# Optimization experiments

Measured on AMD Instinct MI355X. Metric: run time of the kernel, lower is better.

Reference implementation:

```python
import jax, jax.numpy as jnp
import numpy as np

NH, HD = 12, 64          # heads, head dim (d_model=768)
SC = HD ** -0.5          # both Attention and CA_Attention use head_dim**-0.5


def patchify(x, p1, p2):
    # 'b c (h p1) (w p2) -> b (h w) (p1 p2 c)'
    B, C, H, W = x.shape
    h, w = H // p1, W // p2
    x = x.reshape(B, C, h, p1, w, p2).transpose(0, 2, 4, 3, 5, 1)  # b h w p1 p2 c
    return x.reshape(B, h * w, p1 * p2 * C)


def unpatchify(x, h, w, p1, p2, c):
    # 'b (h w) (p1 p2 c) -> b c (h p1) (w p2)'
    B = x.shape[0]
    x = x.reshape(B, h, w, p1, p2, c).transpose(0, 5, 1, 3, 2, 4)
    return x.reshape(B, c, h * p1, w * p2)


def ln(x, g, b):
    m = x.mean(-1, keepdims=True)
    v = ((x - m) ** 2).mean(-1, keepdims=True)
    return (x - m) / jnp.sqrt(v + 1e-5) * g + b


def setup_inputs() -> dict:
    key = jax.random.key(0)
    specs = [
        ('img_feats', (2, 32, 112, 112, 80)), ('txt', (2, 77, 768)),
        ('pe_w_ax', (1120, 768)), ('pe_b_ax', (768,)),
        ('pe_w_sag', (1120, 768)), ('pe_b_sag', (768,)),
        ('pe_w_cor', (1568, 768)), ('pe_b_cor', (768,)),
        ('pos_ax', (1, 256, 768)), ('pos_sag', (1, 256, 768)), ('pos_cor', (1, 256, 768)),
        ('qw', (768, 768)), ('kw', (768, 768)), ('vw', (768, 768)),
        ('pw', (768, 768)), ('pb', (768,)),
        ('caq_w', (768, 768)), ('caq_b', (768,)), ('cak_w', (768, 768)), ('cak_b', (768,)),
        ('cav_w', (768, 768)), ('cav_b', (768,)), ('cao_w', (768, 768)), ('cao_b', (768,)),
        ('mlp_w1', (768, 3072)), ('mlp_b1', (3072,)), ('mlp_w2', (3072, 768)), ('mlp_b2', (768,)),
        ('ow_ax', (768, 1120)), ('ob_ax', (1120,)),
        ('ow_sag', (768, 1120)), ('ob_sag', (1120,)),
        ('ow_cor', (768, 1568)), ('ob_cor', (1568,)),
    ]
    big = {'img_feats', 'txt', 'pos_ax', 'pos_sag', 'pos_cor'}
    out = {}
    for k, (n, s) in zip(jax.random.split(key, len(specs)), specs):
        scale = 1.0 if n in big else 0.02
        out[n] = jax.random.normal(k, s, jnp.float32) * scale
    out['view_w'] = jnp.ones((3,), jnp.float32)
    for n in ('n1_g', 'n2_g', 'n3_g'):
        out[n] = jnp.ones((768,), jnp.float32)
    for n in ('n1_b', 'n2_b', 'n3_b'):
        out[n] = jnp.zeros((768,), jnp.float32)
    return out


def reference(img_feats, txt, pe_w_ax, pe_b_ax, pe_w_sag, pe_b_sag, pe_w_cor, pe_b_cor,
              pos_ax, pos_sag, pos_cor, view_w, qw, kw, vw, pw, pb,
              caq_w, caq_b, cak_w, cak_b, cav_w, cav_b, cao_w, cao_b,
              n1_g, n1_b, n2_g, n2_b, n3_g, n3_b,
              mlp_w1, mlp_b1, mlp_w2, mlp_b2,
              ow_ax, ob_ax, ow_sag, ob_sag, ow_cor, ob_cor):

    def img_attn(t):
        B, N, C = t.shape
        q = (t @ qw).reshape(B, N, NH, HD)
        k = (t @ kw).reshape(B, N, NH, HD)
        v = (t @ vw).reshape(B, N, NH, HD)
        a = jax.nn.softmax(jnp.einsum('bnkc,bmkc->bknm', q, k) * SC, axis=-1)
        x = jnp.einsum('bknm,bmkc->bnkc', a, v).reshape(B, N, C)
        return x @ pw + pb

    def ca_attn(t, im):
        B, T, _ = t.shape
        N = im.shape[1]
        qh = (t @ caq_w + caq_b).reshape(B, T, NH, HD).transpose(0, 2, 1, 3)
        kh = (im @ cak_w + cak_b).reshape(B, N, NH, HD).transpose(0, 2, 1, 3)
        vh = (im @ cav_w + cav_b).reshape(B, N, NH, HD).transpose(0, 2, 1, 3)
        a = jax.nn.softmax(jnp.einsum('bhid,bhjd->bhij', qh, kh) * SC, axis=-1)
        # faithful to original einsum 'b h i j, b h j d -> b h j d' (sums over i)
        o = jnp.einsum('bhij,bhjd->bhjd', a, vh)
        o = o.transpose(0, 2, 1, 3).reshape(B, N, NH * HD)
        return o @ cao_w + cao_b

    def branch(v2d, pe_w, pe_b, pos, ow, ob, p1, p2):
        B, C, H, W = v2d.shape
        h, w = H // p1, W // p2
        q = patchify(v2d, p1, p2) @ pe_w + pe_b + pos
        q = ln(q, n1_g, n1_b)
        q = q + img_attn(q)
        q = ln(q, n2_g, n2_b)
        x = q + ca_attn(txt, q)
        x = x + (jax.nn.gelu(ln(x, n3_g, n3_b) @ mlp_w1 + mlp_b1, approximate=False) @ mlp_w2 + mlp_b2)
        return unpatchify(x @ ow + ob, h, w, p1, p2, C)

    # adaptive_avg_pool3d to size-1 along one axis == mean over that axis
    ax = img_feats.mean(2)    # (B,C,H,W)
    sag = img_feats.mean(3)   # (B,C,D,W)
    cor = img_feats.mean(4)   # (B,C,D,H)
    oax = branch(ax, pe_w_ax, pe_b_ax, pos_ax, ow_ax, ob_ax, 7, 5)
    osag = branch(sag, pe_w_sag, pe_b_sag, pos_sag, ow_sag, ob_sag, 7, 5)
    ocor = branch(cor, pe_w_cor, pe_b_cor, pos_cor, ow_cor, ob_cor, 7, 7)
    v3 = (view_w[0] * oax[:, :, None] + view_w[1] * osag[:, :, :, None]
          + view_w[2] * ocor[:, :, :, :, None])
    return img_feats + v3
```

## Files before the change

### kernel.cpp

```cpp
#include <hip/hip_runtime.h>
#include <math.h>

typedef __attribute__((ext_vector_type(8))) short s8;
typedef __attribute__((ext_vector_type(4))) float f4;
typedef unsigned short u16;

__device__ inline u16 f2bf(float f) {
    unsigned u = __float_as_uint(f);
    u += 0x7fffu + ((u >> 16) & 1u);
    return (u16)(u >> 16);
}
__device__ inline float bf2f(u16 x) {
    return __uint_as_float(((unsigned)x) << 16);
}

__global__ __launch_bounds__(256) void mean3_k(const float* __restrict__ img,
                                               float* __restrict__ axp,
                                               float* __restrict__ sag,
                                               float* __restrict__ cor) {
    __shared__ float sl[112*81];
    int blk = blockIdx.x;
    int dc = blk & 15, bc = blk >> 4;
    int d0 = dc * 7;
    int t = threadIdx.x;
    f4 axr[9];
    #pragma unroll
    for (int k = 0; k < 9; ++k) axr[k] = (f4){0.f,0.f,0.f,0.f};
    const float* base = img + (size_t)bc * 1003520 + (size_t)d0 * 8960;
    for (int sidx = 0; sidx < 7; ++sidx) {
        const f4* sp = reinterpret_cast<const f4*>(base + (size_t)sidx * 8960);
        #pragma unroll
        for (int k = 0; k < 9; ++k) {
            int q = t + k * 256;
            if (q < 2240) {
                f4 v = sp[q];
                axr[k] += v;
                int h = q / 20, w4 = q % 20;
                float* row = &sl[h * 81 + w4 * 4];
                row[0] = v[0]; row[1] = v[1]; row[2] = v[2]; row[3] = v[3];
            }
        }
        __syncthreads();
        if (t < 112) {
            float acc = 0.f;
            #pragma unroll 8
            for (int w = 0; w < 80; ++w) acc += sl[t * 81 + w];
            cor[((size_t)bc * 112 + d0 + sidx) * 112 + t] = acc * (1.f / 80.f);
        } else if (t < 192) {
            int w = t - 112;
            float acc = 0.f;
            #pragma unroll 8
            for (int h = 0; h < 112; ++h) acc += sl[h * 81 + w];
            sag[((size_t)bc * 112 + d0 + sidx) * 80 + w] = acc * (1.f / 112.f);
        }
        __syncthreads();
    }
    float* axo = axp + ((size_t)dc * 64 + bc) * 8960;
    #pragma unroll
    for (int k = 0; k < 9; ++k) {
        int q = t + k * 256;
        if (q < 2240) *reinterpret_cast<f4*>(axo + q * 4) = axr[k];
    }
}

__global__ void axred_k(const float* __restrict__ axp, float* __restrict__ ax) {
    int idx = blockIdx.x * 256 + threadIdx.x;
    if (idx >= 143360) return;
    f4 s = (f4){0.f,0.f,0.f,0.f};
    #pragma unroll
    for (int i = 0; i < 16; ++i)
        s += *reinterpret_cast<const f4*>(axp + (size_t)i * 573440 + (size_t)idx * 4);
    s *= (1.f / 112.f);
    *reinterpret_cast<f4*>(ax + (size_t)idx * 4) = s;
}

struct TT {
    const float* in[16];
    u16* out[16];
    int K[16];
    int N[16];
    int start[16];
};

__global__ __launch_bounds__(256) void transp_all(TT tab) {
    __shared__ float tl[32][33];
    int bid = blockIdx.x;
    int e = 0;
    #pragma unroll
    for (int i = 1; i < 16; ++i) if (bid >= tab.start[i]) e = i;
    const float* in = tab.in[e];
    u16* out = tab.out[e];
    int K = tab.K[e], N = tab.N[e];
    int tid = bid - tab.start[e];
    int nt = N >> 5;
    int k0 = (tid / nt) * 32, n0 = (tid % nt) * 32;
    int t = threadIdx.x;
    int r = t >> 5, c = t & 31;
    #pragma unroll
    for (int i = 0; i < 4; ++i) tl[r + i*8][c] = in[(long)(k0 + r + i*8)*N + n0 + c];
    __syncthreads();
    #pragma unroll
    for (int i = 0; i < 4; ++i) out[(long)(n0 + r + i*8)*K + k0 + c] = f2bf(tl[c][r + i*8]);
}

__global__ void misc_k(const float* __restrict__ txt, u16* __restrict__ txtb,
                       const float* __restrict__ cak_b, const float* __restrict__ cav_b,
                       float* __restrict__ kvb) {
    int idx = blockIdx.x*256 + threadIdx.x;
    if (idx < 118272) { txtb[idx] = f2bf(txt[idx]); return; }
    int i2 = idx - 118272;
    if (i2 < 768) kvb[i2] = cak_b[i2];
    else if (i2 < 1536) kvb[i2] = cav_b[i2 - 768];
}

__global__ __launch_bounds__(256) void patchify3_k(const float* __restrict__ m_ax,
                                                   const float* __restrict__ m_sag,
                                                   const float* __restrict__ m_cor,
                                                   u16* __restrict__ P0, u16* __restrict__ P1,
                                                   u16* __restrict__ P2) {
    __shared__ float sl[32][113];
    int br = blockIdx.y;
    int X = blockIdx.x;
    int b = X / 112, rem = X % 112;
    int hh = rem / 7, pp1 = rem % 7;
    const float* src; u16* dst; int Wt, p2, PD;
    if (br == 0)      { src = m_ax;  dst = P0; Wt = 80;  p2 = 5; PD = 1120; }
    else if (br == 1) { src = m_sag; dst = P1; Wt = 80;  p2 = 5; PD = 1120; }
    else              { src = m_cor; dst = P2; Wt = 112; p2 = 7; PD = 1568; }
    int t = threadIdx.x;
    int row = hh*7 + pp1;
    int wq = Wt >> 2;
    for (int i = t; i < 32*wq; i += 256) {
        int c = i / wq, w4 = i % wq;
        float4 v = *reinterpret_cast<const float4*>(
            src + ((size_t)(b*32 + c)*112 + row)*Wt + w4*4);
        sl[c][w4*4+0] = v.x; sl[c][w4*4+1] = v.y; sl[c][w4*4+2] = v.z; sl[c][w4*4+3] = v.w;
    }
    __syncthreads();
    int tot = 16 * p2 * 32;
    for (int o = t; o < tot; o += 256) {
        int ww = o / (p2*32), rest = o % (p2*32);
        int pp2 = rest >> 5, c = rest & 31;
        dst[((size_t)(b*256 + hh*16 + ww))*PD + (pp1*p2 + pp2)*32 + c]
            = f2bf(sl[c][ww*p2 + pp2]);
    }
}

__device__ inline void load_tile(const u16* __restrict__ P, int ld, int nrows, int K,
                                 int r0, int k0, int t, s8 v[4]) {
    #pragma unroll
    for (int i = 0; i < 4; ++i) {
        int chunk = t + i*256;
        int row = chunk >> 4, c8 = (chunk & 15) * 8;
        s8 x;
        #pragma unroll
        for (int q = 0; q < 8; ++q) x[q] = 0;
        if (r0 + row < nrows && k0 + c8 < K)
            x = *reinterpret_cast<const s8*>(P + (long)(r0 + row)*ld + k0 + c8);
        v[i] = x;
    }
}
__device__ inline void write_tile(u16 (*S)[136], int t, const s8 v[4]) {
    #pragma unroll
    for (int i = 0; i < 4; ++i) {
        int chunk = t + i*256;
        *reinterpret_cast<s8*>(&S[chunk >> 4][(chunk & 15)*8]) = v[i];
    }
}
__device__ inline void mfma_tile(const u16 (*As)[136], const u16 (*Bs)[136],
                                 int wr, int wc, int lane, f4 acc[2][2]) {
    int lrow = lane & 15;
    #pragma unroll
    for (int kh = 0; kh < 4; ++kh) {
        int lk = kh*32 + (lane >> 4) * 8;
        s8 af0 = *reinterpret_cast<const s8*>(&As[wr*32 + lrow][lk]);
        s8 af1 = *reinterpret_cast<const s8*>(&As[wr*32 + 16 + lrow][lk]);
        s8 bg0 = *reinterpret_cast<const s8*>(&Bs[wc*32 + lrow][lk]);
        s8 bg1 = *reinterpret_cast<const s8*>(&Bs[wc*32 + 16 + lrow][lk]);
        acc[0][0] = __builtin_amdgcn_mfma_f32_16x16x32_bf16(af0, bg0, acc[0][0], 0, 0, 0);
        acc[0][1] = __builtin_amdgcn_mfma_f32_16x16x32_bf16(af0, bg1, acc[0][1], 0, 0, 0);
        acc[1][0] = __builtin_amdgcn_mfma_f32_16x16x32_bf16(af1, bg0, acc[1][0], 0, 0, 0);
        acc[1][1] = __builtin_amdgcn_mfma_f32_16x16x32_bf16(af1, bg1, acc[1][1], 0, 0, 0);
    }
}

__global__ __launch_bounds__(256) void gemm_bf(
    const u16* __restrict__ A, const u16* __restrict__ Bt,
    float* __restrict__ Cf, u16* __restrict__ Cb,
    int M, int N, int K, int lda, int ldb, int ldc,
    const float* __restrict__ bias, const float* __restrict__ resid,
    int act, float cscale, int mode)
{
    __shared__ u16 As[2][64][136];
    __shared__ u16 Bs[2][64][136];
    const u16* Ab = A;
    const u16* Bb = Bt;
    long coff = 0;
    int z = blockIdx.z;
    if (mode == 1) {
        long o = (long)(z / 12) * 256 * lda + (long)(z % 12) * 64;
        Ab += o; Bb += o; coff = (long)z * 256 * ldc;
    } else if (mode == 2) {
        Ab += (long)z * 65536; Bb += (long)z * 16384;
        coff = (long)(z / 12) * 256 * ldc + (long)(z % 12) * 64;
    } else if (mode == 3) {
        int rowblk = z / 12, h = z % 12;
        Ab += (long)(rowblk & 1) * 77 * lda + (long)h * 64;
        Bb += (long)rowblk * 256 * ldb + (long)h * 64;
        coff = (long)z * 77 * 256;
    }
    int t = threadIdx.x;
    int m0 = blockIdx.y * 64, n0 = blockIdx.x * 64;
    int wave = t >> 6, lane = t & 63;
    int wr = wave >> 1, wc = wave & 1;
    f4 acc[2][2];
    #pragma unroll
    for (int m = 0; m < 2; ++m)
        #pragma unroll
        for (int n = 0; n < 2; ++n)
            #pragma unroll
            for (int r = 0; r < 4; ++r) acc[m][n][r] = 0.f;
    int nk = (K + 127) >> 7;
    s8 pa[4], pbv[4];
    load_tile(Ab, lda, M, K, m0, 0, t, pa);
    load_tile(Bb, ldb, N, K, n0, 0, t, pbv);
    write_tile(As[0], t, pa);
    write_tile(Bs[0], t, pbv);
    __syncthreads();
    for (int kt = 0; kt < nk; ++kt) {
        int cur = kt & 1;
        if (kt + 1 < nk) {
            load_tile(Ab, lda, M, K, m0, (kt+1) << 7, t, pa);
            load_tile(Bb, ldb, N, K, n0, (kt+1) << 7, t, pbv);
        }
        mfma_tile(As[cur], Bs[cur], wr, wc, lane, acc);
        if (kt + 1 < nk) {
            write_tile(As[cur^1], t, pa);
            write_tile(Bs[cur^1], t, pbv);
        }
        __syncthreads();
    }
    #pragma unroll
    for (int m = 0; m < 2; ++m) {
        int rbase = m0 + wr*32 + m*16 + (lane >> 4) * 4;
        #pragma unroll
        for (int n = 0; n < 2; ++n) {
            int col = n0 + wc*32 + n*16 + (lane & 15);
            if (col >= N) continue;
            #pragma unroll
            for (int r = 0; r < 4; ++r) {
                int row = rbase + r;
                if (row >= M) continue;
                float v = acc[m][n][r];
                if (bias)  v += bias[col];
                if (resid) v += resid[(long)row * ldc + col];
                if (act == 1) v = 0.5f * v * (1.0f + erff(v * 0.70710678118654752f));
                v *= cscale;
                long ci = coff + (long)row * ldc + col;
                if (Cf) Cf[ci] = v;
                if (Cb) Cb[ci] = f2bf(v);
            }
        }
    }
}

struct PeDesc {
    const u16* A[3];
    const u16* Bt[3];
    const float* bias[3];
    const float* pos[3];
    int K[3];
};

__global__ __launch_bounds__(256) void gemm_pe(PeDesc d, float* __restrict__ C) {
    __shared__ u16 As[2][64][136];
    __shared__ u16 Bs[2][64][136];
    int z = blockIdx.z;
    const u16* Ab = d.A[z];
    const u16* Bb = d.Bt[z];
    const float* bias = d.bias[z];
    const float* pos = d.pos[z];
    int K = d.K[z];
    int t = threadIdx.x;
    int m0 = blockIdx.y * 64, n0 = blockIdx.x * 64;
    int wave = t >> 6, lane = t & 63;
    int wr = wave >> 1, wc = wave & 1;
    f4 acc[2][2];
    #pragma unroll
    for (int m = 0; m < 2; ++m)
        #pragma unroll
        for (int n = 0; n < 2; ++n)
            #pragma unroll
            for (int r = 0; r < 4; ++r) acc[m][n][r] = 0.f;
    int nk = (K + 127) >> 7;
    s8 pa[4], pbv[4];
    load_tile(Ab, K, 512, K, m0, 0, t, pa);
    load_tile(Bb, K, 768, K, n0, 0, t, pbv);
    write_tile(As[0], t, pa);
    write_tile(Bs[0], t, pbv);
    __syncthreads();
    for (int kt = 0; kt < nk; ++kt) {
        int cur = kt & 1;
        if (kt + 1 < nk) {
            load_tile(Ab, K, 512, K, m0, (kt+1) << 7, t, pa);
            load_tile(Bb, K, 768, K, n0, (kt+1) << 7, t, pbv);
        }
        mfma_tile(As[cur], Bs[cur], wr, wc, lane, acc);
        if (kt + 1 < nk) {
            write_tile(As[cur^1], t, pa);
            write_tile(Bs[cur^1], t, pbv);
        }
        __syncthreads();
    }
    float* Cz = C + (long)z * 512 * 768;
    #pragma unroll
    for (int m = 0; m < 2; ++m) {
        int rbase = m0 + wr*32 + m*16 + (lane >> 4) * 4;
        #pragma unroll
        for (int n = 0; n < 2; ++n) {
            int col = n0 + wc*32 + n*16 + (lane & 15);
            #pragma unroll
            for (int r = 0; r < 4; ++r) {
                int row = rbase + r;
                float v = acc[m][n][r] + bias[col] + pos[(long)(row & 255)*768 + col];
                Cz[(long)row * 768 + col] = v;
            }
        }
    }
}

struct OwDesc {
    const u16* Bt[3];
    float* C[3];
    const float* bias[3];
    int N[3];
};

__global__ __launch_bounds__(256) void gemm_ow(OwDesc d, const u16* __restrict__ A) {
    int z = blockIdx.z;
    int N = d.N[z];
    int n0 = blockIdx.x * 64;
    if (n0 >= N) return;
    __shared__ u16 As[2][64][136];
    __shared__ u16 Bs[2][64][136];
    const u16* Ab = A + (long)z * 512 * 768;
    const u16* Bb = d.Bt[z];
    int t = threadIdx.x;
    int m0 = blockIdx.y * 64;
    int wave = t >> 6, lane = t & 63;
    int wr = wave >> 1, wc = wave & 1;
    f4 acc[2][2];
    #pragma unroll
    for (int m = 0; m < 2; ++m)
        #pragma unroll
        for (int n = 0; n < 2; ++n)
            #pragma unroll
            for (int r = 0; r < 4; ++r) acc[m][n][r] = 0.f;
    s8 pa[4], pbv[4];
    load_tile(Ab, 768, 512, 768, m0, 0, t, pa);
    load_tile(Bb, 768, N, 768, n0, 0, t, pbv);
    write_tile(As[0], t, pa);
    write_tile(Bs[0], t, pbv);
    __syncthreads();
    for (int kt = 0; kt < 6; ++kt) {
        int cur = kt & 1;
        if (kt + 1 < 6) {
            load_tile(Ab, 768, 512, 768, m0, (kt+1) << 7, t, pa);
            load_tile(Bb, 768, N, 768, n0, (kt+1) << 7, t, pbv);
        }
        mfma_tile(As[cur], Bs[cur], wr, wc, lane, acc);
        if (kt + 1 < 6) {
            write_tile(As[cur^1], t, pa);
            write_tile(Bs[cur^1], t, pbv);
        }
        __syncthreads();
    }
    float* Cz = d.C[z];
    const float* bias = d.bias[z];
    #pragma unroll
    for (int m = 0; m < 2; ++m) {
        int rbase = m0 + wr*32 + m*16 + (lane >> 4) * 4;
        #pragma unroll
        for (int n = 0; n < 2; ++n) {
            int col = n0 + wc*32 + n*16 + (lane & 15);
            if (col >= N) continue;
            #pragma unroll
            for (int r = 0; r < 4; ++r) {
                int row = rbase + r;
                Cz[(long)row * N + col] = acc[m][n][r] + bias[col];
            }
        }
    }
}

__global__ __launch_bounds__(256) void ln_k(const float* __restrict__ in,
                                            float* __restrict__ outf,
                                            u16* __restrict__ outb,
                                            const float* __restrict__ g,
                                            const float* __restrict__ bta) {
    constexpr int N = 768;
    int row = blockIdx.x;
    const float* x = in + (size_t)row * N;
    int t = threadIdx.x;
    float v0 = x[t], v1 = x[t+256], v2 = x[t+512];
    float s = v0+v1+v2, s2 = v0*v0+v1*v1+v2*v2;
    #pragma unroll
    for (int off = 32; off > 0; off >>= 1) { s += __shfl_down(s, off); s2 += __shfl_down(s2, off); }
    __shared__ float red[8];
    int wid = t >> 6, lane = t & 63;
    if (lane == 0) { red[wid] = s; red[wid+4] = s2; }
    __syncthreads();
    if (t == 0) {
        float S = red[0]+red[1]+red[2]+red[3];
        float S2 = red[4]+red[5]+red[6]+red[7];
        float mean = S * (1.f/N);
        float var = S2 * (1.f/N) - mean*mean;
        red[0] = mean; red[1] = rsqrtf(var + 1e-5f);
    }
    __syncthreads();
    float mean = red[0], rstd = red[1];
    float y0 = (v0-mean)*rstd*g[t]     + bta[t];
    float y1 = (v1-mean)*rstd*g[t+256] + bta[t+256];
    float y2 = (v2-mean)*rstd*g[t+512] + bta[t+512];
    if (outf) {
        float* y = outf + (size_t)row * N;
        y[t] = y0; y[t+256] = y1; y[t+512] = y2;
    }
    if (outb) {
        u16* y = outb + (size_t)row * N;
        y[t] = f2bf(y0); y[t+256] = f2bf(y1); y[t+512] = f2bf(y2);
    }
}

__global__ void vt_k(const u16* __restrict__ QKV, u16* __restrict__ Vt) {
    int idx = blockIdx.x*256 + threadIdx.x;
    if (idx >= 72*64*256) return;
    int j = idx & 255, rest = idx >> 8;
    int d = rest & 63, z = rest >> 6;
    Vt[idx] = QKV[((long)(z/12)*256 + j)*2304 + 1536 + (long)(z%12)*64 + d];
}

__global__ __launch_bounds__(256) void softmax_k(const float* __restrict__ S,
                                                 u16* __restrict__ P) {
    int row = blockIdx.x*4 + (threadIdx.x >> 6);
    int lane = threadIdx.x & 63;
    const float4 v = *reinterpret_cast<const float4*>(S + (long)row*256 + lane*4);
    float m = fmaxf(fmaxf(v.x, v.y), fmaxf(v.z, v.w));
    #pragma unroll
    for (int o = 32; o; o >>= 1) m = fmaxf(m, __shfl_xor(m, o));
    float p0 = __expf(v.x - m), p1 = __expf(v.y - m), p2 = __expf(v.z - m), p3 = __expf(v.w - m);
    float l = p0 + p1 + p2 + p3;
    #pragma unroll
    for (int o = 32; o; o >>= 1) l += __shfl_xor(l, o);
    float inv = 1.f / l;
    unsigned b0 = f2bf(p0*inv), b1 = f2bf(p1*inv), b2 = f2bf(p2*inv), b3 = f2bf(p3*inv);
    uint2 pk; pk.x = b0 | (b1 << 16); pk.y = b2 | (b3 << 16);
    *reinterpret_cast<uint2*>(P + (long)row*256 + lane*4) = pk;
}

__global__ __launch_bounds__(256) void ca_cs_k(const float* __restrict__ S2,
                                               float* __restrict__ W) {
    __shared__ float sl[4*256];
    int bh = blockIdx.x;
    int t = threadIdx.x;
    int w = t >> 6, lane = t & 63;
    float wacc[4] = {0.f, 0.f, 0.f, 0.f};
    for (int i = w; i < 77; i += 4) {
        const float4 v = *reinterpret_cast<const float4*>(S2 + ((long)bh*77 + i)*256 + lane*4);
        float m = fmaxf(fmaxf(v.x, v.y), fmaxf(v.z, v.w));
        #pragma unroll
        for (int o = 32; o; o >>= 1) m = fmaxf(m, __shfl_xor(m, o));
        float p0 = __expf(v.x - m), p1 = __expf(v.y - m), p2 = __expf(v.z - m), p3 = __expf(v.w - m);
        float l = p0 + p1 + p2 + p3;
        #pragma unroll
        for (int o = 32; o; o >>= 1) l += __shfl_xor(l, o);
        float inv = 1.f / l;
        wacc[0] += p0*inv; wacc[1] += p1*inv; wacc[2] += p2*inv; wacc[3] += p3*inv;
    }
    #pragma unroll
    for (int k = 0; k < 4; ++k) sl[w*256 + lane*4 + k] = wacc[k];
    __syncthreads();
    W[(long)bh*256 + t] = sl[t] + sl[256 + t] + sl[512 + t] + sl[768 + t];
}

__global__ void ca_apply_k(const float* __restrict__ W, const u16* __restrict__ KVHb,
                           u16* __restrict__ O) {
    int idx = blockIdx.x*256 + threadIdx.x;
    if (idx >= 1536*768) return;
    int row = idx / 768, col = idx - row*768;
    int rowblk = row >> 8, j = row & 255, h = col >> 6;
    float vh = bf2f(KVHb[(long)row*1536 + 768 + col]);
    O[idx] = f2bf(W[((long)rowblk*12 + h)*256 + j] * vh);
}

__global__ void unpatch3_k(const float* __restrict__ Y0, const float* __restrict__ Y1,
                           const float* __restrict__ Y2, const float* __restrict__ vw,
                           float* __restrict__ Aax, float* __restrict__ Asag,
                           float* __restrict__ Acor) {
    int idx = blockIdx.x*256 + threadIdx.x;
    if (idx >= 1949696) return;
    const float* y; float* A; float wt; int Wd, p2, PD, p;
    if (idx < 573440)       { y = Y0; A = Aax;  wt = vw[0]; Wd = 80;  p2 = 5; PD = 1120; p = idx; }
    else if (idx < 1146880) { y = Y1; A = Asag; wt = vw[1]; Wd = 80;  p2 = 5; PD = 1120; p = idx - 573440; }
    else                    { y = Y2; A = Acor; wt = vw[2]; Wd = 112; p2 = 7; PD = 1568; p = idx - 1146880; }
    int w = p % Wd; int r = p / Wd;
    int h = r % 112; r /= 112;
    int c = r % 32; int b = r / 32;
    int src = (b*256 + (h/7)*16 + (w/p2))*PD + ((h%7)*p2 + (w%p2))*32 + c;
    A[p] = wt * y[src];
}

__global__ __launch_bounds__(256) void final_k(const float* __restrict__ img,
                                               const float* __restrict__ Aax,
                                               const float* __restrict__ Asag,
                                               const float* __restrict__ Acor,
                                               float* __restrict__ out) {
    int blk = blockIdx.x;
    int bc = blk / 112;
    const float4* ip = reinterpret_cast<const float4*>(img + (size_t)blk * 8960);
    const float4* ap = reinterpret_cast<const float4*>(Aax + (size_t)bc * 8960);
    const float4* sp = reinterpret_cast<const float4*>(Asag + (size_t)blk * 80);
    const float*  cp = Acor + (size_t)blk * 112;
    float4* op = reinterpret_cast<float4*>(out + (size_t)blk * 8960);
    int t = threadIdx.x;
    for (int q = t; q < 2240; q += 256) {
        int h = q / 20, w4 = q % 20;
        float4 iv = ip[q], av = ap[q], sv = sp[w4];
        float cv = cp[h];
        float4 o;
        o.x = iv.x + av.x + sv.x + cv;
        o.y = iv.y + av.y + sv.y + cv;
        o.z = iv.z + av.z + sv.z + cv;
        o.w = iv.w + av.w + sv.w + cv;
        op[q] = o;
    }
}

extern "C" void kernel_launch(void* const* d_in, const int* in_sizes, int n_in,
                              void* d_out, int out_size, void* d_ws, size_t ws_size,
                              hipStream_t stream) {
    (void)in_sizes; (void)n_in; (void)out_size; (void)ws_size;
    const float* img    = (const float*)d_in[0];
    const float* txt    = (const float*)d_in[1];
    const float* pe_w[3] = {(const float*)d_in[2], (const float*)d_in[4], (const float*)d_in[6]};
    const float* pe_b[3] = {(const float*)d_in[3], (const float*)d_in[5], (const float*)d_in[7]};
    const float* pos[3]  = {(const float*)d_in[8], (const float*)d_in[9], (const float*)d_in[10]};
    const float* qw = (const float*)d_in[11];
    const float* kw = (const float*)d_in[12];
    const float* vw_attn = (const float*)d_in[13];
    const float* pw = (const float*)d_in[14];
    const float* pb = (const float*)d_in[15];
    const float* caq_w = (const float*)d_in[16];
    const float* caq_b = (const float*)d_in[17];
    const float* cak_w = (const float*)d_in[18];
    const float* cak_b = (const float*)d_in[19];
    const float* cav_w = (const float*)d_in[20];
    const float* cav_b = (const float*)d_in[21];
    const float* cao_w = (const float*)d_in[22];
    const float* cao_b = (const float*)d_in[23];
    const float* mlp_w1 = (const float*)d_in[24];
    const float* mlp_b1 = (const float*)d_in[25];
    const float* mlp_w2 = (const float*)d_in[26];
    const float* mlp_b2 = (const float*)d_in[27];
    const float* ow[3] = {(const float*)d_in[28], (const float*)d_in[30], (const float*)d_in[32]};
    const float* ob[3] = {(const float*)d_in[29], (const float*)d_in[31], (const float*)d_in[33]};
    const float* view_w = (const float*)d_in[34];
    const float* n_g[3] = {(const float*)d_in[35], (const float*)d_in[36], (const float*)d_in[37]};
    const float* n_b[3] = {(const float*)d_in[38], (const float*)d_in[39], (const float*)d_in[40]};

    unsigned char* sb = (unsigned char*)d_out;
    size_t off = 0;
    auto B = [&](size_t bytes) -> void* {
        void* p = sb + off; off += (bytes + 511) & ~(size_t)511; return p;
    };
    u16* qkvT  = (u16*)B((size_t)2304*768*2);
    u16* pwT   = (u16*)B(768*768*2);
    u16* caqT  = (u16*)B(768*768*2);
    u16* cakvT = (u16*)B((size_t)1536*768*2);
    u16* caoT  = (u16*)B(768*768*2);
    u16* mlp1T = (u16*)B((size_t)3072*768*2);
    u16* mlp2T = (u16*)B((size_t)768*3072*2);
    u16* peT[3]; peT[0] = (u16*)B((size_t)768*1120*2); peT[1] = (u16*)B((size_t)768*1120*2); peT[2] = (u16*)B((size_t)768*1568*2);
    u16* owT[3]; owT[0] = (u16*)B((size_t)1120*768*2); owT[1] = (u16*)B((size_t)1120*768*2); owT[2] = (u16*)B((size_t)1568*768*2);
    u16* txtb = (u16*)B(154*768*2);
    float* kvb = (float*)B(1536*4);
    float* axp   = (float*)B((size_t)16*573440*4);
    float* m_ax  = (float*)B(573440*4);
    float* m_sag = (float*)B(573440*4);
    float* m_cor = (float*)B(802816*4);
    u16* P0 = (u16*)B((size_t)512*1120*2);
    u16* P1 = (u16*)B((size_t)512*1120*2);
    u16* P2 = (u16*)B((size_t)512*1568*2);
    float* X0  = (float*)B((size_t)1536*768*4);
    float* X1f = (float*)B((size_t)1536*768*4);
    float* X2  = (float*)B((size_t)1536*768*4);
    float* X3f = (float*)B((size_t)1536*768*4);
    float* X4  = (float*)B((size_t)1536*768*4);
    u16* X1b = (u16*)B((size_t)1536*768*2);
    u16* X3b = (u16*)B((size_t)1536*768*2);
    u16* X5b = (u16*)B((size_t)1536*768*2);
    u16* X6b = (u16*)B((size_t)1536*768*2);
    u16* QKVb = (u16*)B((size_t)1536*2304*2);
    u16* Obf = (u16*)B((size_t)1536*768*2);
    u16* Vt  = (u16*)B((size_t)72*64*256*2);
    u16* Hb  = (u16*)B((size_t)1536*3072*2);
    float* S  = (float*)B((size_t)72*256*256*4);
    u16* Pat = (u16*)B((size_t)72*256*256*2);
    u16* KVHb = (u16*)B((size_t)1536*1536*2);
    u16* QHb  = (u16*)B((size_t)154*768*2);
    float* S2 = (float*)B((size_t)72*77*256*4);
    float* Wb = (float*)B((size_t)72*256*4);
    float* Y[3];
    Y[0] = (float*)B(573440*4);
    Y[1] = (float*)B(573440*4);
    Y[2] = (float*)B(802816*4);

    float* ws = (float*)d_ws;
    float* Aax  = ws;
    float* Asag = ws + 573440;
    float* Acor = ws + 1146880;

    TT tab;
    {
        const float* ins[16] = {qw, kw, vw_attn, pw, caq_w, cak_w, cav_w, cao_w,
                                mlp_w1, mlp_w2, pe_w[0], pe_w[1], pe_w[2], ow[0], ow[1], ow[2]};
        u16* outs[16] = {qkvT, qkvT + 768*768, qkvT + 2*768*768, pwT, caqT, cakvT,
                         cakvT + 768*768, caoT, mlp1T, mlp2T, peT[0], peT[1], peT[2],
                         owT[0], owT[1], owT[2]};
        int Ks[16] = {768,768,768,768,768,768,768,768, 768,3072, 1120,1120,1568, 768,768,768};
        int Ns[16] = {768,768,768,768,768,768,768,768, 3072,768, 768,768,768, 1120,1120,1568};
        int st = 0;
        for (int i = 0; i < 16; ++i) {
            tab.in[i] = ins[i]; tab.out[i] = outs[i]; tab.K[i] = Ks[i]; tab.N[i] = Ns[i];
            tab.start[i] = st;
            st += (Ks[i] >> 5) * (Ns[i] >> 5);
        }
        transp_all<<<st, 256, 0, stream>>>(tab);
    }
    misc_k<<<468, 256, 0, stream>>>(txt, txtb, cak_b, cav_b, kvb);

    mean3_k<<<1024, 256, 0, stream>>>(img, axp, m_sag, m_cor);
    axred_k<<<560, 256, 0, stream>>>(axp, m_ax);
    patchify3_k<<<dim3(224,3), 256, 0, stream>>>(m_ax, m_sag, m_cor, P0, P1, P2);

    auto gemm = [&](const u16* A, const u16* Bt, float* Cf, u16* Cb,
                    int M, int N, int K, int lda, int ldb, int ldc,
                    const float* bias, const float* resid,
                    int act, float cscale, int mode, int batch) {
        dim3 g((N+63)/64, (M+63)/64, batch);
        gemm_bf<<<g, 256, 0, stream>>>(A, Bt, Cf, Cb, M, N, K, lda, ldb, ldc,
                                       bias, resid, act, cscale, mode);
    };

    gemm(txtb, caqT, nullptr, QHb, 154, 768, 768, 768, 768, 768,
         caq_b, nullptr, 0, 1.f, 0, 1);

    {
        PeDesc d;
        d.A[0] = P0; d.A[1] = P1; d.A[2] = P2;
        d.Bt[0] = peT[0]; d.Bt[1] = peT[1]; d.Bt[2] = peT[2];
        d.bias[0] = pe_b[0]; d.bias[1] = pe_b[1]; d.bias[2] = pe_b[2];
        d.pos[0] = pos[0]; d.pos[1] = pos[1]; d.pos[2] = pos[2];
        d.K[0] = 1120; d.K[1] = 1120; d.K[2] = 1568;
        gemm_pe<<<dim3(12,8,3), 256, 0, stream>>>(d, X0);
    }

    ln_k<<<1536, 256, 0, stream>>>(X0, X1f, X1b, n_g[0], n_b[0]);
    gemm(X1b, qkvT, nullptr, QKVb, 1536, 2304, 768, 768, 768, 2304,
         nullptr, nullptr, 0, 1.f, 0, 1);
    vt_k<<<4608, 256, 0, stream>>>(QKVb, Vt);
    gemm(QKVb, QKVb + 768, S, nullptr, 256, 256, 64, 2304, 2304, 256,
         nullptr, nullptr, 0, 0.125f, 1, 72);
    softmax_k<<<4608, 256, 0, stream>>>(S, Pat);
    gemm(Pat, Vt, nullptr, Obf, 256, 64, 256, 256, 256, 768,
         nullptr, nullptr, 0, 1.f, 2, 72);
    gemm(Obf, pwT, X2, nullptr, 1536, 768, 768, 768, 768, 768, pb, X1f, 0, 1.f, 0, 1);
    ln_k<<<1536, 256, 0, stream>>>(X2, X3f, X3b, n_g[1], n_b[1]);
    gemm(X3b, cakvT, nullptr, KVHb, 1536, 1536, 768, 768, 768, 1536,
         kvb, nullptr, 0, 1.f, 0, 1);
    gemm(QHb, KVHb, S2, nullptr, 77, 256, 64, 768, 1536, 256,
         nullptr, nullptr, 0, 0.125f, 3, 72);
    ca_cs_k<<<72, 256, 0, stream>>>(S2, Wb);
    ca_apply_k<<<4608, 256, 0, stream>>>(Wb, KVHb, Obf);
    gemm(Obf, caoT, X4, nullptr, 1536, 768, 768, 768, 768, 768, cao_b, X3f, 0, 1.f, 0, 1);
    ln_k<<<1536, 256, 0, stream>>>(X4, nullptr, X5b, n_g[2], n_b[2]);
    gemm(X5b, mlp1T, nullptr, Hb, 1536, 3072, 768, 768, 768, 3072, mlp_b1, nullptr, 1, 1.f, 0, 1);
    gemm(Hb, mlp2T, nullptr, X6b, 1536, 768, 3072, 3072, 3072, 768, mlp_b2, X4, 0, 1.f, 0, 1);
    {
        OwDesc d;
        d.Bt[0] = owT[0]; d.Bt[1] = owT[1]; d.Bt[2] = owT[2];
        d.C[0] = Y[0]; d.C[1] = Y[1]; d.C[2] = Y[2];
        d.bias[0] = ob[0]; d.bias[1] = ob[1]; d.bias[2] = ob[2];
        d.N[0] = 1120; d.N[1] = 1120; d.N[2] = 1568;
        gemm_ow<<<dim3(25,8,3), 256, 0, stream>>>(d, X6b);
    }

    unpatch3_k<<<7616, 256, 0, stream>>>(Y[0], Y[1], Y[2], view_w, Aax, Asag, Acor);
    final_k<<<7168, 256, 0, stream>>>(img, Aax, Asag, Acor, (float*)d_out);
}
```

Baseline: 493.1 us.

## Add 128x128 bf16 MFMA GEMM with fused V-transpose and merge CA kernels

Adds a 128x128-tile, double-buffered bf16 MFMA GEMM for the large projections (QKV, cross-attn KV, MLP up with GELU). In the QKV case its epilogue also writes the transposed V, which removes the separate vt_k pass. The cross-attention column-sum and apply kernels are merged into one kernel that keeps the weights in shared memory, removing a launch and a global round trip. The risks are the 72-block ca_k underfilling the GPU, the uncoalesced scattered Vt stores, and the larger tiles lowering occupancy.

```diff
diff --git a/kernel.cpp b/kernel.cpp
--- a/kernel.cpp
+++ b/kernel.cpp
@@ -264,6 +264,101 @@
     }
 }
 
+__global__ __launch_bounds__(256) void gemm_big(
+    const u16* __restrict__ A, const u16* __restrict__ Bt,
+    u16* __restrict__ Cb, u16* __restrict__ vt,
+    int N, int K,
+    const float* __restrict__ bias, int act)
+{
+    __shared__ u16 As[2][128][72];
+    __shared__ u16 Bs[2][128][72];
+    int t = threadIdx.x;
+    int m0 = blockIdx.y * 128, n0 = blockIdx.x * 128;
+    int wave = t >> 6, lane = t & 63;
+    int wr = wave >> 1, wc = wave & 1;
+    f4 acc[4][4];
+    #pragma unroll
+    for (int m = 0; m < 4; ++m)
+        #pragma unroll
+        for (int n = 0; n < 4; ++n)
+            #pragma unroll
+            for (int r = 0; r < 4; ++r) acc[m][n][r] = 0.f;
+    int nk = K >> 6;
+    s8 pa[4], pbv[4];
+    #pragma unroll
+    for (int i = 0; i < 4; ++i) {
+        int chunk = t + i*256;
+        pa[i]  = *reinterpret_cast<const s8*>(A  + (long)(m0 + (chunk>>3))*K + (chunk&7)*8);
+        pbv[i] = *reinterpret_cast<const s8*>(Bt + (long)(n0 + (chunk>>3))*K + (chunk&7)*8);
+    }
+    #pragma unroll
+    for (int i = 0; i < 4; ++i) {
+        int chunk = t + i*256;
+        *reinterpret_cast<s8*>(&As[0][chunk>>3][(chunk&7)*8]) = pa[i];
+        *reinterpret_cast<s8*>(&Bs[0][chunk>>3][(chunk&7)*8]) = pbv[i];
+    }
+    __syncthreads();
+    for (int kt = 0; kt < nk; ++kt) {
+        int cur = kt & 1;
+        if (kt + 1 < nk) {
+            int k0 = (kt+1) << 6;
+            #pragma unroll
+            for (int i = 0; i < 4; ++i) {
+                int chunk = t + i*256;
+                pa[i]  = *reinterpret_cast<const s8*>(A  + (long)(m0 + (chunk>>3))*K + k0 + (chunk&7)*8);
+                pbv[i] = *reinterpret_cast<const s8*>(Bt + (long)(n0 + (chunk>>3))*K + k0 + (chunk&7)*8);
+            }
+        }
+        #pragma unroll
+        for (int kh = 0; kh < 2; ++kh) {
+            int lk = kh*32 + (lane >> 4) * 8;
+            int lr = lane & 15;
+            s8 af[4], bf[4];
+            #pragma unroll
+            for (int m = 0; m < 4; ++m)
+                af[m] = *reinterpret_cast<const s8*>(&As[cur][wr*64 + m*16 + lr][lk]);
+            #pragma unroll
+            for (int n = 0; n < 4; ++n)
+                bf[n] = *reinterpret_cast<const s8*>(&Bs[cur][wc*64 + n*16 + lr][lk]);
+            #pragma unroll
+            for (int m = 0; m < 4; ++m)
+                #pragma unroll
+                for (int n = 0; n < 4; ++n)
+                    acc[m][n] = __builtin_amdgcn_mfma_f32_16x16x32_bf16(af[m], bf[n], acc[m][n], 0, 0, 0);
+        }
+        if (kt + 1 < nk) {
+            #pragma unroll
+            for (int i = 0; i < 4; ++i) {
+                int chunk = t + i*256;
+                *reinterpret_cast<s8*>(&As[cur^1][chunk>>3][(chunk&7)*8]) = pa[i];
+                *reinterpret_cast<s8*>(&Bs[cur^1][chunk>>3][(chunk&7)*8]) = pbv[i];
+            }
+        }
+        __syncthreads();
+    }
+    #pragma unroll
+    for (int m = 0; m < 4; ++m) {
+        int rbase = m0 + wr*64 + m*16 + (lane >> 4) * 4;
+        #pragma unroll
+        for (int n = 0; n < 4; ++n) {
+            int col = n0 + wc*64 + n*16 + (lane & 15);
+            #pragma unroll
+            for (int r = 0; r < 4; ++r) {
+                int row = rbase + r;
+                float v = acc[m][n][r];
+                if (bias) v += bias[col];
+                if (act == 1) v = 0.5f * v * (1.0f + erff(v * 0.70710678118654752f));
+                u16 b = f2bf(v);
+                Cb[(long)row * N + col] = b;
+                if (vt && col >= 1536) {
+                    int z = (row >> 8) * 12 + ((col - 1536) >> 6);
+                    vt[((long)z * 64 + (col & 63)) * 256 + (row & 255)] = b;
+                }
+            }
+        }
+    }
+}
+
 struct PeDesc {
     const u16* A[3];
     const u16* Bt[3];
@@ -432,14 +527,6 @@
     }
 }
 
-__global__ void vt_k(const u16* __restrict__ QKV, u16* __restrict__ Vt) {
-    int idx = blockIdx.x*256 + threadIdx.x;
-    if (idx >= 72*64*256) return;
-    int j = idx & 255, rest = idx >> 8;
-    int d = rest & 63, z = rest >> 6;
-    Vt[idx] = QKV[((long)(z/12)*256 + j)*2304 + 1536 + (long)(z%12)*64 + d];
-}
-
 __global__ __launch_bounds__(256) void softmax_k(const float* __restrict__ S,
                                                  u16* __restrict__ P) {
     int row = blockIdx.x*4 + (threadIdx.x >> 6);
@@ -458,10 +545,13 @@
     *reinterpret_cast<uint2*>(P + (long)row*256 + lane*4) = pk;
 }
 
-__global__ __launch_bounds__(256) void ca_cs_k(const float* __restrict__ S2,
-                                               float* __restrict__ W) {
+__global__ __launch_bounds__(256) void ca_k(const float* __restrict__ S2,
+                                            const u16* __restrict__ KVHb,
+                                            u16* __restrict__ O) {
     __shared__ float sl[4*256];
+    __shared__ float wj[256];
     int bh = blockIdx.x;
+    int rowblk = bh / 12, h = bh % 12;
     int t = threadIdx.x;
     int w = t >> 6, lane = t & 63;
     float wacc[4] = {0.f, 0.f, 0.f, 0.f};
@@ -480,17 +570,16 @@
     #pragma unroll
     for (int k = 0; k < 4; ++k) sl[w*256 + lane*4 + k] = wacc[k];
     __syncthreads();
-    W[(long)bh*256 + t] = sl[t] + sl[256 + t] + sl[512 + t] + sl[768 + t];
-}
-
-__global__ void ca_apply_k(const float* __restrict__ W, const u16* __restrict__ KVHb,
-                           u16* __restrict__ O) {
-    int idx = blockIdx.x*256 + threadIdx.x;
-    if (idx >= 1536*768) return;
-    int row = idx / 768, col = idx - row*768;
-    int rowblk = row >> 8, j = row & 255, h = col >> 6;
-    float vh = bf2f(KVHb[(long)row*1536 + 768 + col]);
-    O[idx] = f2bf(W[((long)rowblk*12 + h)*256 + j] * vh);
+    wj[t] = sl[t] + sl[256 + t] + sl[512 + t] + sl[768 + t];
+    __syncthreads();
+    int d = t & 63;
+    #pragma unroll 4
+    for (int it = 0; it < 64; ++it) {
+        int j = it*4 + (t >> 6);
+        long row = (long)rowblk*256 + j;
+        float vh = bf2f(KVHb[row*1536 + 768 + h*64 + d]);
+        O[row*768 + h*64 + d] = f2bf(wj[j] * vh);
+    }
 }
 
 __global__ void unpatch3_k(const float* __restrict__ Y0, const float* __restrict__ Y1,
@@ -609,7 +698,6 @@
     u16* KVHb = (u16*)B((size_t)1536*1536*2);
     u16* QHb  = (u16*)B((size_t)154*768*2);
     float* S2 = (float*)B((size_t)72*77*256*4);
-    float* Wb = (float*)B((size_t)72*256*4);
     float* Y[3];
     Y[0] = (float*)B(573440*4);
     Y[1] = (float*)B(573440*4);
@@ -666,9 +754,7 @@
     }
 
     ln_k<<<1536, 256, 0, stream>>>(X0, X1f, X1b, n_g[0], n_b[0]);
-    gemm(X1b, qkvT, nullptr, QKVb, 1536, 2304, 768, 768, 768, 2304,
-         nullptr, nullptr, 0, 1.f, 0, 1);
-    vt_k<<<4608, 256, 0, stream>>>(QKVb, Vt);
+    gemm_big<<<dim3(18,12), 256, 0, stream>>>(X1b, qkvT, QKVb, Vt, 2304, 768, nullptr, 0);
     gemm(QKVb, QKVb + 768, S, nullptr, 256, 256, 64, 2304, 2304, 256,
          nullptr, nullptr, 0, 0.125f, 1, 72);
     softmax_k<<<4608, 256, 0, stream>>>(S, Pat);
@@ -676,15 +762,13 @@
          nullptr, nullptr, 0, 1.f, 2, 72);
     gemm(Obf, pwT, X2, nullptr, 1536, 768, 768, 768, 768, 768, pb, X1f, 0, 1.f, 0, 1);
     ln_k<<<1536, 256, 0, stream>>>(X2, X3f, X3b, n_g[1], n_b[1]);
-    gemm(X3b, cakvT, nullptr, KVHb, 1536, 1536, 768, 768, 768, 1536,
-         kvb, nullptr, 0, 1.f, 0, 1);
+    gemm_big<<<dim3(12,12), 256, 0, stream>>>(X3b, cakvT, KVHb, nullptr, 1536, 768, kvb, 0);
     gemm(QHb, KVHb, S2, nullptr, 77, 256, 64, 768, 1536, 256,
          nullptr, nullptr, 0, 0.125f, 3, 72);
-    ca_cs_k<<<72, 256, 0, stream>>>(S2, Wb);
-    ca_apply_k<<<4608, 256, 0, stream>>>(Wb, KVHb, Obf);
+    ca_k<<<72, 256, 0, stream>>>(S2, KVHb, Obf);
     gemm(Obf, caoT, X4, nullptr, 1536, 768, 768, 768, 768, 768, cao_b, X3f, 0, 1.f, 0, 1);
     ln_k<<<1536, 256, 0, stream>>>(X4, nullptr, X5b, n_g[2], n_b[2]);
-    gemm(X5b, mlp1T, nullptr, Hb, 1536, 3072, 768, 768, 768, 3072, mlp_b1, nullptr, 1, 1.f, 0, 1);
+    gemm_big<<<dim3(24,12), 256, 0, stream>>>(X5b, mlp1T, Hb, nullptr, 3072, 768, mlp_b1, 1);
     gemm(Hb, mlp2T, nullptr, X6b, 1536, 768, 3072, 3072, 3072, 768, mlp_b2, X4, 0, 1.f, 0, 1);
     {
         OwDesc d;
```

Result: no change. 489.0 us (-0.8%).
